# Performance work log

Hardware: AMD Instinct MI355X
Metric: run time of the kernel (lower is better)

## Reference

```python
import jax, jax.numpy as jnp
import numpy as np

N_STREAMS = 4
SINKHORN_ITERS = 20
EPS = 1e-8


def sinkhorn_knopp(log_mat, num_iters=SINKHORN_ITERS, eps=EPS):
    mat = jnp.exp(log_mat)
    def body(_, m):
        m = m / (m.sum(axis=-2, keepdims=True) + eps)
        m = m / (m.sum(axis=-1, keepdims=True) + eps)
        return m
    return jax.lax.fori_loop(0, num_iters, body, mat)


def setup_inputs() -> dict:
    key = jax.random.key(0)
    B, L, C = 4, 2048, 1024
    n = N_STREAMS
    hidden = 4 * C
    ks = jax.random.split(key, 8)
    def xavier(k, shape):
        fan_in, fan_out = shape[0], shape[1]
        lim = np.sqrt(6.0 / (fan_in + fan_out))
        return jax.random.uniform(k, shape, jnp.float32, -lim, lim)
    return {
        "x": jax.random.normal(ks[0], (B, L, C), jnp.float32),
        "rms_weight": jnp.ones((C * n,), jnp.float32),
        "W_dyn": xavier(ks[1], (C * n, n * n + 2 * n)),  # Linear no-bias, stored [in,out]
        "bias_pre": jnp.zeros((1, n), jnp.float32),
        "bias_post": jnp.zeros((1, n), jnp.float32),
        "bias_res": jnp.zeros((n, n), jnp.float32),
        "alpha_pre": jnp.full((1,), 0.01, jnp.float32),
        "alpha_post": jnp.full((1,), 0.01, jnp.float32),
        "alpha_res": jnp.full((1,), 0.01, jnp.float32),
        "W1": xavier(ks[2], (C, hidden)),
        "b1": jnp.zeros((hidden,), jnp.float32),
        "W2": xavier(ks[3], (hidden, C)),
        "b2": jnp.zeros((C,), jnp.float32),
        "Wout": xavier(ks[4], (C * n, C)),
        "bout": jnp.zeros((C,), jnp.float32),
    }


def reference(x, rms_weight, W_dyn, bias_pre, bias_post, bias_res,
              alpha_pre, alpha_post, alpha_res, W1, b1, W2, b2, Wout, bout):
    B, L, C = x.shape
    n = bias_pre.shape[1]
    # x expanded across streams (broadcast view, no copy)
    x_exp = jnp.broadcast_to(x[:, :, None, :], (B, L, n, C))  # [B,L,n,C]
    x_flat = x_exp.reshape(B, L, n * C)
    # RMSNorm
    rms = jnp.sqrt(jnp.mean(x_flat * x_flat, axis=-1, keepdims=True) + EPS)
    x_norm = x_flat / rms * rms_weight
    # dynamic projection
    dynamic = x_norm @ W_dyn  # [B,L,n*n+2n]
    dyn_pre = dynamic[..., :n]
    dyn_post = dynamic[..., n:2 * n]
    dyn_res = dynamic[..., 2 * n:].reshape(B, L, n, n)
    H_pre = jax.nn.sigmoid(alpha_pre * dyn_pre + bias_pre)            # [B,L,n]
    H_post = 2.0 * jax.nn.sigmoid(alpha_post * dyn_post + bias_post)  # [B,L,n]
    H_res = sinkhorn_knopp(alpha_res * dyn_res + bias_res)            # [B,L,n,n]
    # pre-mix streams then residual MLP
    pre_mixed = jnp.einsum('bln,blnc->blc', H_pre, x_exp)
    h = jax.nn.gelu(pre_mixed @ W1 + b1, approximate=False)
    f_out = h @ W2 + b2  # [B,L,C]
    # post mixing + doubly-stochastic residual mixing
    post_mixed = H_post[..., None] * f_out[:, :, None, :]             # [B,L,n,C]
    res_mixed = jnp.einsum('blnm,blmc->blnc', H_res, x_exp)
    merged = (res_mixed + post_mixed).reshape(B, L, n * C)
    return merged @ Wout + bout + x
```

## Files before the change

kernel.cpp:

```cpp
#include <hip/hip_runtime.h>

typedef unsigned short u16;
typedef __bf16 bf16x8 __attribute__((ext_vector_type(8)));
typedef float f32x4 __attribute__((ext_vector_type(4)));

__device__ __forceinline__ u16 f2bf(float f) {
  unsigned int u = __builtin_bit_cast(unsigned int, f);
  u += 0x7fffu + ((u >> 16) & 1u);
  return (u16)(u >> 16);
}

__device__ __forceinline__ void gload_lds16(const u16* g, u16* l) {
  __builtin_amdgcn_global_load_lds((const __attribute__((address_space(1))) unsigned int*)g,
                                   (__attribute__((address_space(3))) unsigned int*)l,
                                   16, 0, 0);
}

__device__ __forceinline__ float gelu_erf(float v) {
  const float z = v * 0.70710678118654752f;
  const float az = fabsf(z);
  const float t = __builtin_amdgcn_rcpf(1.0f + 0.3275911f * az);
  const float p = t * (0.254829592f +
                  t * (-0.284496736f +
                  t * (1.421413741f +
                  t * (-1.453152027f + t * 1.061405429f))));
  const float e = __expf(-az * az);
  float er = 1.0f - p * e;
  er = (z < 0.f) ? -er : er;
  return 0.5f * v * (1.0f + er);
}


__global__ __launch_bounds__(256) void weff_kernel(const float* __restrict__ rmsw,
                                                   const float* __restrict__ Wdyn,
                                                   float* __restrict__ WT) {
  int idx = blockIdx.x * 256 + threadIdx.x;
  int j = idx >> 10, c = idx & 1023;
  float s = 0.f;
#pragma unroll
  for (int st = 0; st < 4; ++st) {
    int r = st * 1024 + c;
    s += rmsw[r] * Wdyn[(long)r * 24 + j];
  }
  WT[idx] = s;
}

__global__ __launch_bounds__(256) void pack_all(const float* __restrict__ W1,
                                                const float* __restrict__ W2,
                                                const float* __restrict__ WO,
                                                u16* __restrict__ F1,
                                                u16* __restrict__ F2,
                                                u16* __restrict__ FO) {
  const int blk = blockIdx.x;
  const int sel = blk >> 11;
  const float* W;
  u16* FMB;
  int lgN, KC;
  if (sel == 0)      { W = W1; FMB = F1; lgN = 12; KC = 32; }
  else if (sel == 1) { W = W2; FMB = F2; lgN = 10; KC = 128; }
  else               { W = WO; FMB = FO; lgN = 10; KC = 128; }
  const long gid = (long)(blk & 2047) * 256 + threadIdx.x;
  const int N = 1 << lgN;
  const int n = (int)(gid & (N - 1));
  const int k0 = (int)(gid >> lgN) * 8;
  unsigned int p[4];
#pragma unroll
  for (int d = 0; d < 4; ++d) {
    const float lo = W[(long)(k0 + 2 * d) * N + n];
    const float hi = W[(long)(k0 + 2 * d + 1) * N + n];
    p[d] = (unsigned)f2bf(lo) | ((unsigned)f2bf(hi) << 16);
  }
  const long ad = ((long)(n >> 4) * KC + (k0 >> 5)) * 512 +
                  ((n & 15) + (((k0 >> 3) & 3) << 4)) * 8;
  *(uint4*)(FMB + ad) = make_uint4(p[0], p[1], p[2], p[3]);
}

__global__ __launch_bounds__(512) void prep_tokens(
    const float* __restrict__ x, const float* __restrict__ WT,
    const float* __restrict__ bias_pre, const float* __restrict__ bias_post,
    const float* __restrict__ bias_res, const float* __restrict__ a_pre,
    const float* __restrict__ a_post, const float* __restrict__ a_res,
    u16* __restrict__ preA, float* __restrict__ scal) {
  const int tid = threadIdx.x;
  const int b = blockIdx.x;
  const long t0 = (long)b * 16;

  __shared__ float smem[24 * 1024];
  __shared__ float tot2[16][26];
  __shared__ float spre[16];

#pragma unroll
  for (int q = 0; q < 12; ++q) {
    const int o = (q * 512 + tid) * 4;
    *(float4*)(smem + o) = *(const float4*)(WT + o);
  }
  __syncthreads();

  float part[25];
  {
    const int tt = tid & 15;
    const int cc = tid >> 4;
    const float* xp = x + (t0 + tt) * 1024 + cc * 32;
#pragma unroll
    for (int j = 0; j < 25; ++j) part[j] = 0.f;
#pragma unroll
    for (int g = 0; g < 8; ++g) {
      const float4 xv = *(const float4*)(xp + g * 4);
      part[24] += xv.x * xv.x + xv.y * xv.y + xv.z * xv.z + xv.w * xv.w;
#pragma unroll
      for (int j = 0; j < 24; ++j) {
        const float4 wv = *(const float4*)(smem + j * 1024 + cc * 32 + g * 4);
        part[j] += xv.x * wv.x + xv.y * wv.y + xv.z * wv.z + xv.w * wv.w;
      }
    }
  }
  __syncthreads();
  float (*red)[16][26] = (float(*)[16][26])smem;
  {
    const int tt = tid & 15;
    const int cc = tid >> 4;
#pragma unroll
    for (int j = 0; j < 25; ++j) red[cc][tt][j] = part[j];
  }
  __syncthreads();

  {
    const int tt = tid >> 5;
    const int j = tid & 31;
    if (j < 25) {
      float s = 0.f;
#pragma unroll
      for (int cc = 0; cc < 32; ++cc) s += red[cc][tt][j];
      tot2[tt][j] = s;
    }
  }
  __syncthreads();

  if (tid < 256) {
    const int tt = tid >> 4;
    const int m = tid & 15;
    const long t = t0 + tt;
    const float rms = sqrtf(tot2[tt][24] * (1.0f / 1024.0f) + 1e-8f);
    const float rinv = 1.0f / rms;

    if (m == 0) {
      const float ap = a_pre[0];
      float s_pre = 0.f;
#pragma unroll
      for (int i = 0; i < 4; ++i)
        s_pre += 1.f / (1.f + expf(-(ap * tot2[tt][i] * rinv + bias_pre[i])));
      spre[tt] = s_pre;
    }
    if (m < 4) {
      const float apo = a_post[0];
      float hp = 2.f / (1.f + expf(-(apo * tot2[tt][4 + m] * rinv + bias_post[m])));
      scal[t * 8 + 4 + m] = hp;
    }
    const float ar = a_res[0];
    float Mv = expf(ar * tot2[tt][8 + m] * rinv + bias_res[m]);
#pragma unroll
    for (int it = 0; it < 20; ++it) {
      float cs = Mv + __shfl_xor(Mv, 4);
      cs += __shfl_xor(cs, 8);
      Mv = Mv / (cs + 1e-8f);
      float rs = Mv + __shfl_xor(Mv, 1);
      rs += __shfl_xor(rs, 2);
      Mv = Mv / (rs + 1e-8f);
    }
    float rs = Mv + __shfl_xor(Mv, 1);
    rs += __shfl_xor(rs, 2);
    if ((m & 3) == 0) scal[t * 8 + (m >> 2)] = rs;
  }
  __syncthreads();

  {
    const int w = tid >> 6;
    const int lane = tid & 63;
    const int tl = lane & 15;
    const int co = (lane >> 4) * 8;
    const float sp = spre[tl];
#pragma unroll
    for (int p = 0; p < 4; ++p) {
      const int ki = p * 8 + w;
      const float* xr = x + (t0 + tl) * 1024 + ki * 32 + co;
      const float4 xa = *(const float4*)(xr);
      const float4 xb = *(const float4*)(xr + 4);
      unsigned q0 = (unsigned)f2bf(sp * xa.x) | ((unsigned)f2bf(sp * xa.y) << 16);
      unsigned q1 = (unsigned)f2bf(sp * xa.z) | ((unsigned)f2bf(sp * xa.w) << 16);
      unsigned q2 = (unsigned)f2bf(sp * xb.x) | ((unsigned)f2bf(sp * xb.y) << 16);
      unsigned q3 = (unsigned)f2bf(sp * xb.z) | ((unsigned)f2bf(sp * xb.w) << 16);
      *(uint4*)(preA + ((long)b * 32 + ki) * 512 + lane * 8) = make_uint4(q0, q1, q2, q3);
    }
  }
}

template <int EPI, int NT, int SWZ, int LGGX>
__global__ __launch_bounds__(512, 2) void gemm_fm2(const u16* __restrict__ A,
                                                   const u16* __restrict__ B,
                                                   const int KCtot, const int KCout,
                                                   const float* __restrict__ bias,
                                                   const float* __restrict__ X,
                                                   const float* __restrict__ scal,
                                                   void* __restrict__ dstv) {
  constexpr int CH = 16 + NT;
  constexpr int SC = CH / 8;
  constexpr int AI = (NT == 16) ? 8 : 4;
  const int tid = threadIdx.x;
  const int lane = tid & 63;
  const int wave = tid >> 6;
  const int wm = (NT == 16) ? (wave >> 2) : (wave >> 1);
  const int wn = (NT == 16) ? (wave & 3) : (wave & 1);
  const int b = blockIdx.x;
  int bx, by;
  if constexpr (SWZ == 1) {
    const int c = b & 7, u = b >> 3;
    const int p = u >> 5, v = u & 31;
    by = (p * 2 + (c >> 2)) * 4 + (v >> 3);
    bx = (c & 3) * 8 + (v & 7);
  } else {
    const int c = b & 7, s = b >> 3;
    bx = s & ((1 << LGGX) - 1);
    by = c * 4 + (s >> LGGX);
  }

  __shared__ u16 lds[4][CH][512];
  u16* const l0 = (u16*)lds;

  const u16* gb[4];
#pragma unroll
  for (int l = 0; l < SC; ++l) {
    const int t = wave * SC + l;
    gb[l] = (t < 16) ? (A + ((long)(by * 16 + t) * KCtot) * 512 + lane * 8)
                     : (B + ((long)(bx * NT + (t - 16)) * KCtot) * 512 + lane * 8);
  }

#define STG(kt)                                                              \
  {                                                                          \
    u16* cb_ = l0 + (((kt) & 3) * CH + wave * SC) * 512;                     \
    const long ko_ = (long)(kt)*512;                                         \
    _Pragma("unroll") for (int l_ = 0; l_ < SC; ++l_)                        \
        gload_lds16(gb[l_] + ko_, cb_ + l_ * 512);                           \
  }

  f32x4 acc[AI][4] = {};

  STG(0); STG(1); STG(2);
  if constexpr (SC == 4) asm volatile("s_waitcnt vmcnt(8)" ::: "memory");
  else                   asm volatile("s_waitcnt vmcnt(6)" ::: "memory");
  __builtin_amdgcn_s_barrier();

  for (int kt = 0; kt < KCtot; ++kt) {
    if (kt + 3 < KCtot) STG(kt + 3);
    const u16* cb = l0 + (kt & 3) * (CH * 512);
    bf16x8 af[AI], bf[4];
#pragma unroll
    for (int i = 0; i < AI; ++i)
      af[i] = *(const bf16x8*)(cb + (wm * AI + i) * 512 + lane * 8);
#pragma unroll
    for (int j = 0; j < 4; ++j)
      bf[j] = *(const bf16x8*)(cb + (16 + wn * 4 + j) * 512 + lane * 8);
    asm volatile("s_waitcnt lgkmcnt(0)" ::: "memory");
    __builtin_amdgcn_sched_barrier(0);
    __builtin_amdgcn_s_setprio(1);
#pragma unroll
    for (int i = 0; i < AI; ++i)
#pragma unroll
      for (int j = 0; j < 4; ++j)
        acc[i][j] = __builtin_amdgcn_mfma_f32_16x16x32_bf16(af[i], bf[j], acc[i][j], 0, 0, 0);
    __builtin_amdgcn_s_setprio(0);
    if (kt + 4 <= KCtot) {
      if constexpr (SC == 4) asm volatile("s_waitcnt vmcnt(8)" ::: "memory");
      else                   asm volatile("s_waitcnt vmcnt(6)" ::: "memory");
    } else if (kt + 3 == KCtot) {
      if constexpr (SC == 4) asm volatile("s_waitcnt vmcnt(4)" ::: "memory");
      else                   asm volatile("s_waitcnt vmcnt(3)" ::: "memory");
    } else {
      asm volatile("s_waitcnt vmcnt(0)" ::: "memory");
    }
    __builtin_amdgcn_s_barrier();
  }
#undef STG

  if constexpr (EPI == 0) {
    u16* dst = (u16*)dstv;
    u16* ep = l0 + wave * (2 * AI * 512);
#pragma unroll
    for (int i = 0; i < AI; ++i)
#pragma unroll
      for (int j = 0; j < 4; ++j) {
        const int col = bx * (NT * 16) + wn * 64 + j * 16 + (lane & 15);
        const float bcol = bias[col];
#pragma unroll
        for (int r = 0; r < 4; ++r) {
          const float g = gelu_erf(acc[i][j][r] + bcol);
          const int lp = ((lane >> 4) * 4 + r) | ((((j & 1) << 1) | ((lane & 15) >> 3)) << 4);
          ep[(i * 2 + (j >> 1)) * 512 + lp * 8 + (lane & 7)] = f2bf(g);
        }
      }
#pragma unroll
    for (int ch = 0; ch < 2 * AI; ++ch) {
      const int i = ch >> 1, jc = ch & 1;
      const long row16 = by * 16 + wm * AI + i;
      const long col32 = bx * (NT / 2) + wn * 2 + jc;
      *(uint4*)(dst + (row16 * KCout + col32) * 512 + lane * 8) =
          *(const uint4*)(ep + ch * 512 + lane * 8);
    }
  } else if constexpr (EPI == 1) {
    u16* dst = (u16*)dstv;
    u16* ep = l0 + wave * 4096;
#pragma unroll
    for (int i = 0; i < AI; ++i) {
      float rr[4][4], hh[4][4];
#pragma unroll
      for (int r = 0; r < 4; ++r) {
        const int row = by * 256 + wm * 64 + i * 16 + (lane >> 4) * 4 + r;
        const float4 rv = *(const float4*)(scal + (long)row * 8);
        const float4 hv = *(const float4*)(scal + (long)row * 8 + 4);
        rr[r][0] = rv.x; rr[r][1] = rv.y; rr[r][2] = rv.z; rr[r][3] = rv.w;
        hh[r][0] = hv.x; hh[r][1] = hv.y; hh[r][2] = hv.z; hh[r][3] = hv.w;
      }
#pragma unroll
      for (int jc = 0; jc < 2; ++jc) {
#pragma unroll
        for (int jj = 0; jj < 2; ++jj) {
          const int j = jc * 2 + jj;
          const int col = bx * 128 + wn * 64 + j * 16 + (lane & 15);
          const float bcol = bias[col];
#pragma unroll
          for (int r = 0; r < 4; ++r) {
            const int row = by * 256 + wm * 64 + i * 16 + (lane >> 4) * 4 + r;
            const float f = acc[i][j][r] + bcol;
            const float xval = X[(long)row * 1024 + col];
            const int lp = ((lane >> 4) * 4 + r) | (((jj << 1) | ((lane & 15) >> 3)) << 4);
#pragma unroll
            for (int ss = 0; ss < 4; ++ss)
              ep[ss * 512 + lp * 8 + (lane & 7)] = f2bf(rr[r][ss] * xval + hh[r][ss] * f);
          }
        }
        const long row16 = by * 16 + wm * 4 + i;
        const long col32 = bx * 4 + wn * 2 + jc;
#pragma unroll
        for (int ss = 0; ss < 4; ++ss)
          *(uint4*)(dst + (row16 * 128 + (long)ss * 32 + col32) * 512 + lane * 8) =
              *(const uint4*)(ep + ss * 512 + lane * 8);
      }
    }
  } else {
    float* dst = (float*)dstv;
    float* ep32 = (float*)(l0 + wave * 4096);
#pragma unroll
    for (int half = 0; half < 2; ++half) {
#pragma unroll
      for (int i2 = 0; i2 < 2; ++i2) {
        const int i = half * 2 + i2;
#pragma unroll
        for (int j = 0; j < 4; ++j) {
          const int col = bx * 128 + wn * 64 + j * 16 + (lane & 15);
          const float bcol = bias[col];
#pragma unroll
          for (int r = 0; r < 4; ++r) {
            const long row = by * 256 + wm * 64 + i * 16 + (lane >> 4) * 4 + r;
            ep32[(i2 * 16 + (lane >> 4) * 4 + r) * 64 + j * 16 + (lane & 15)] =
                acc[i][j][r] + bcol + X[row * 1024 + col];
          }
        }
      }
#pragma unroll
      for (int q = 0; q < 8; ++q) {
        const int lr = q * 4 + (lane >> 4);
        const long row = by * 256 + wm * 64 + half * 32 + lr;
        const long col = bx * 128 + wn * 64 + (lane & 15) * 4;
        *(float4*)(dst + row * 1024 + col) =
            *(const float4*)(ep32 + lr * 64 + (lane & 15) * 4);
      }
    }
  }
}

extern "C" void kernel_launch(void* const* d_in, const int* in_sizes, int n_in,
                              void* d_out, int out_size, void* d_ws, size_t ws_size,
                              hipStream_t stream) {
  (void)in_sizes; (void)n_in; (void)out_size; (void)ws_size;
  const float* x = (const float*)d_in[0];
  const float* rmsw = (const float*)d_in[1];
  const float* Wdyn = (const float*)d_in[2];
  const float* bias_pre = (const float*)d_in[3];
  const float* bias_post = (const float*)d_in[4];
  const float* bias_res = (const float*)d_in[5];
  const float* a_pre = (const float*)d_in[6];
  const float* a_post = (const float*)d_in[7];
  const float* a_res = (const float*)d_in[8];
  const float* W1 = (const float*)d_in[9];
  const float* b1 = (const float*)d_in[10];
  const float* W2 = (const float*)d_in[11];
  const float* b2 = (const float*)d_in[12];
  const float* Wout = (const float*)d_in[13];
  const float* bout = (const float*)d_in[14];
  float* out = (float*)d_out;
  char* ws = (char*)d_ws;

  constexpr size_t MB = 1048576;
  u16* W1fm = (u16*)(ws);
  u16* W2fm = (u16*)(ws + 8 * MB);
  u16* WOfm = (u16*)(ws + 16 * MB);
  float* WT = (float*)(ws + 24 * MB);
  float* scal = (float*)(ws + 24 * MB + 98304);
  u16* h = (u16*)(ws + 25 * MB);
  u16* merged = (u16*)(ws + 89 * MB);
  u16* preA = (u16*)(ws + 89 * MB);

  weff_kernel<<<96, 256, 0, stream>>>(rmsw, Wdyn, WT);
  pack_all<<<6144, 256, 0, stream>>>(W1, W2, Wout, W1fm, W2fm, WOfm);
  prep_tokens<<<512, 512, 0, stream>>>(x, WT, bias_pre, bias_post, bias_res,
                                       a_pre, a_post, a_res, preA, scal);
  gemm_fm2<0, 8, 1, 0><<<1024, 512, 0, stream>>>(preA, W1fm, 32, 128, b1, nullptr, nullptr, h);
  gemm_fm2<1, 8, 0, 3><<<256, 512, 0, stream>>>(h, W2fm, 128, 128, b2, x, scal, merged);
  gemm_fm2<2, 8, 0, 3><<<256, 512, 0, stream>>>(merged, WOfm, 128, 0, bout, x, nullptr, out);
}
```

Measured before the change: 428.0 us.

## Add dedicated 128x128-tile GEMM for W1 and drop LDS staging in prep_tokens

Replaces the generic 256-row-tile GEMM used for the first MLP layer (K=1024) with a dedicated 256-thread kernel that uses 128x128 output tiles, a 4-deep LDS ring buffer, and a grouped block-index swizzle. This doubles the grid to 2048 blocks for better occupancy and balance on the short-K GEMM, at the cost of less reuse per tile. prep_tokens also stops copying the 96KB projection weight into shared memory and reads it directly from global/L2, which cuts LDS usage but puts more load traffic on the cache.

Result: no change. 426.0 us (-0.5%).

```diff
diff --git a/kernel.cpp b/kernel.cpp
--- a/kernel.cpp
+++ b/kernel.cpp
@@ -85,22 +85,15 @@
   const int b = blockIdx.x;
   const long t0 = (long)b * 16;
 
-  __shared__ float smem[24 * 1024];
+  __shared__ float red[32][16][26];
   __shared__ float tot2[16][26];
   __shared__ float spre[16];
 
-#pragma unroll
-  for (int q = 0; q < 12; ++q) {
-    const int o = (q * 512 + tid) * 4;
-    *(float4*)(smem + o) = *(const float4*)(WT + o);
-  }
-  __syncthreads();
-
-  float part[25];
   {
     const int tt = tid & 15;
     const int cc = tid >> 4;
     const float* xp = x + (t0 + tt) * 1024 + cc * 32;
+    float part[25];
 #pragma unroll
     for (int j = 0; j < 25; ++j) part[j] = 0.f;
 #pragma unroll
@@ -109,16 +102,10 @@
       part[24] += xv.x * xv.x + xv.y * xv.y + xv.z * xv.z + xv.w * xv.w;
 #pragma unroll
       for (int j = 0; j < 24; ++j) {
-        const float4 wv = *(const float4*)(smem + j * 1024 + cc * 32 + g * 4);
+        const float4 wv = *(const float4*)(WT + (long)j * 1024 + cc * 32 + g * 4);
         part[j] += xv.x * wv.x + xv.y * wv.y + xv.z * wv.z + xv.w * wv.w;
       }
     }
-  }
-  __syncthreads();
-  float (*red)[16][26] = (float(*)[16][26])smem;
-  {
-    const int tt = tid & 15;
-    const int cc = tid >> 4;
 #pragma unroll
     for (int j = 0; j < 25; ++j) red[cc][tt][j] = part[j];
   }
@@ -191,6 +178,95 @@
       unsigned q3 = (unsigned)f2bf(sp * xb.z) | ((unsigned)f2bf(sp * xb.w) << 16);
       *(uint4*)(preA + ((long)b * 32 + ki) * 512 + lane * 8) = make_uint4(q0, q1, q2, q3);
     }
+  }
+}
+
+__global__ __launch_bounds__(256, 2) void gemm_fm1(const u16* __restrict__ A,
+                                                   const u16* __restrict__ B,
+                                                   const float* __restrict__ bias,
+                                                   u16* __restrict__ dst) {
+  const int tid = threadIdx.x;
+  const int lane = tid & 63;
+  const int wave = tid >> 6;
+  const int wm = wave >> 1, wn = wave & 1;
+  const int b = blockIdx.x;
+  const int c = b & 7, u = b >> 3;
+  const int p = u >> 5, v = u & 31;
+  const int by = (p * 2 + (c >> 2)) * 4 + (v >> 3);
+  const int bx = (c & 3) * 8 + (v & 7);
+
+  __shared__ u16 lds[4][16][512];
+  u16* const l0 = (u16*)lds;
+
+  const u16* gb[4];
+#pragma unroll
+  for (int l = 0; l < 4; ++l) {
+    const int t = wave * 4 + l;
+    gb[l] = (t < 8) ? (A + ((long)(by * 8 + t) * 32) * 512 + lane * 8)
+                    : (B + ((long)(bx * 8 + (t - 8)) * 32) * 512 + lane * 8);
+  }
+
+#define STG(kt)                                                              \
+  {                                                                          \
+    u16* cb_ = l0 + (((kt) & 3) * 16 + wave * 4) * 512;                      \
+    const long ko_ = (long)(kt)*512;                                         \
+    _Pragma("unroll") for (int l_ = 0; l_ < 4; ++l_)                         \
+        gload_lds16(gb[l_] + ko_, cb_ + l_ * 512);                           \
+  }
+
+  f32x4 acc[4][4] = {};
+
+  STG(0); STG(1); STG(2);
+  asm volatile("s_waitcnt vmcnt(8)" ::: "memory");
+  __builtin_amdgcn_s_barrier();
+
+  for (int kt = 0; kt < 32; ++kt) {
+    if (kt + 3 < 32) STG(kt + 3);
+    const u16* cb = l0 + (kt & 3) * (16 * 512);
+    bf16x8 af[4], bf[4];
+#pragma unroll
+    for (int i = 0; i < 4; ++i)
+      af[i] = *(const bf16x8*)(cb + (wm * 4 + i) * 512 + lane * 8);
+#pragma unroll
+    for (int j = 0; j < 4; ++j)
+      bf[j] = *(const bf16x8*)(cb + (8 + wn * 4 + j) * 512 + lane * 8);
+    asm volatile("s_waitcnt lgkmcnt(0)" ::: "memory");
+    __builtin_amdgcn_sched_barrier(0);
+    __builtin_amdgcn_s_setprio(1);
+#pragma unroll
+    for (int i = 0; i < 4; ++i)
+#pragma unroll
+      for (int j = 0; j < 4; ++j)
+        acc[i][j] = __builtin_amdgcn_mfma_f32_16x16x32_bf16(af[i], bf[j], acc[i][j], 0, 0, 0);
+    __builtin_amdgcn_s_setprio(0);
+    if (kt + 4 <= 32)      asm volatile("s_waitcnt vmcnt(8)" ::: "memory");
+    else if (kt + 3 == 32) asm volatile("s_waitcnt vmcnt(4)" ::: "memory");
+    else                   asm volatile("s_waitcnt vmcnt(0)" ::: "memory");
+    __builtin_amdgcn_s_barrier();
+  }
+#undef STG
+
+  u16* ep = l0 + wave * 4096;
+#pragma unroll
+  for (int i = 0; i < 4; ++i)
+#pragma unroll
+    for (int j = 0; j < 4; ++j) {
+      const int col = bx * 128 + wn * 64 + j * 16 + (lane & 15);
+      const float bcol = bias[col];
+#pragma unroll
+      for (int r = 0; r < 4; ++r) {
+        const float g = gelu_erf(acc[i][j][r] + bcol);
+        const int lp = ((lane >> 4) * 4 + r) | ((((j & 1) << 1) | ((lane & 15) >> 3)) << 4);
+        ep[(i * 2 + (j >> 1)) * 512 + lp * 8 + (lane & 7)] = f2bf(g);
+      }
+    }
+#pragma unroll
+  for (int ch = 0; ch < 8; ++ch) {
+    const int i = ch >> 1, jc = ch & 1;
+    const long row16 = by * 8 + wm * 4 + i;
+    const long col32 = bx * 4 + wn * 2 + jc;
+    *(uint4*)(dst + (row16 * 128 + col32) * 512 + lane * 8) =
+        *(const uint4*)(ep + ch * 512 + lane * 8);
   }
 }
 
@@ -281,31 +357,7 @@
   }
 #undef STG
 
-  if constexpr (EPI == 0) {
-    u16* dst = (u16*)dstv;
-    u16* ep = l0 + wave * (2 * AI * 512);
-#pragma unroll
-    for (int i = 0; i < AI; ++i)
-#pragma unroll
-      for (int j = 0; j < 4; ++j) {
-        const int col = bx * (NT * 16) + wn * 64 + j * 16 + (lane & 15);
-        const float bcol = bias[col];
-#pragma unroll
-        for (int r = 0; r < 4; ++r) {
-          const float g = gelu_erf(acc[i][j][r] + bcol);
-          const int lp = ((lane >> 4) * 4 + r) | ((((j & 1) << 1) | ((lane & 15) >> 3)) << 4);
-          ep[(i * 2 + (j >> 1)) * 512 + lp * 8 + (lane & 7)] = f2bf(g);
-        }
-      }
-#pragma unroll
-    for (int ch = 0; ch < 2 * AI; ++ch) {
-      const int i = ch >> 1, jc = ch & 1;
-      const long row16 = by * 16 + wm * AI + i;
-      const long col32 = bx * (NT / 2) + wn * 2 + jc;
-      *(uint4*)(dst + (row16 * KCout + col32) * 512 + lane * 8) =
-          *(const uint4*)(ep + ch * 512 + lane * 8);
-    }
-  } else if constexpr (EPI == 1) {
+  if constexpr (EPI == 1) {
     u16* dst = (u16*)dstv;
     u16* ep = l0 + wave * 4096;
 #pragma unroll
@@ -413,7 +465,7 @@
   pack_all<<<6144, 256, 0, stream>>>(W1, W2, Wout, W1fm, W2fm, WOfm);
   prep_tokens<<<512, 512, 0, stream>>>(x, WT, bias_pre, bias_post, bias_res,
                                        a_pre, a_post, a_res, preA, scal);
-  gemm_fm2<0, 8, 1, 0><<<1024, 512, 0, stream>>>(preA, W1fm, 32, 128, b1, nullptr, nullptr, h);
+  gemm_fm1<<<2048, 256, 0, stream>>>(preA, W1fm, b1, h);
   gemm_fm2<1, 8, 0, 3><<<256, 512, 0, stream>>>(h, W2fm, 128, 128, b2, x, scal, merged);
   gemm_fm2<2, 8, 0, 3><<<256, 512, 0, stream>>>(merged, WOfm, 128, 0, bout, x, nullptr, out);
 }
```
